# Performance work log

Hardware: AMD Instinct MI355X
Metric: run time of the kernel (lower is better)

The kernel has to match this reference:

```python
import jax, jax.numpy as jnp
import numpy as np

RADIUS = 5
KERNEL = 2 * RADIUS + 1  # 11
N_PATCHES = KERNEL * KERNEL  # 121
SIGMA_DIAG = np.array([10.0, 10.0, 0.02, 0.02, 0.02, 0.1, 0.1, 0.1], dtype=np.float32)


def _shift(x):
    # x: [B, C, H, W] -> [B, P, C, H, W] with P = KERNEL^2 reflect-padded window shifts
    b, c, h, w = x.shape
    xp = jnp.pad(x, ((0, 0), (0, 0), (RADIUS, RADIUS), (RADIUS, RADIUS)), mode='reflect')
    patches = [xp[:, :, dy:dy + h, dx:dx + w]
               for dy in range(KERNEL) for dx in range(KERNEL)]
    return jnp.stack(patches, axis=1)


def setup_inputs() -> dict:
    key = jax.random.key(0)
    k1, k2 = jax.random.split(key)
    image = jax.random.uniform(k1, (2, 3, 256, 256), dtype=jnp.float32)
    guidance = jax.random.uniform(k2, (2, 8, 256, 256), dtype=jnp.float32)
    return {"image": image, "guidance": guidance}


def reference(image, guidance):
    # sigma_inv = inverse of diag(SIGMA_DIAG): diagonal, so just reciprocal per channel
    sigma_inv = jnp.asarray(1.0 / SIGMA_DIAG, dtype=guidance.dtype)  # [8]

    sg = _shift(guidance)                       # [B, P, 8, H, W]
    center = sg[:, N_PATCHES // 2:N_PATCHES // 2 + 1]
    diff = sg - center                          # [B, P, 8, H, W]
    # Mahalanobis^2 with diagonal sigma_inv: sum_c diff^2 / sigma_c
    maha_sq = jnp.einsum('bpchw,c->bphw', diff * diff, sigma_inv)
    weights = jnp.exp(-0.5 * maha_sq)           # [B, P, H, W]

    si = _shift(image)                          # [B, P, 3, H, W]
    weighted_sum = jnp.einsum('bpchw,bphw->bchw', si, weights)
    sum_w = jnp.clip(jnp.sum(weights, axis=1, keepdims=False), 1e-10, None)  # [B, H, W]
    return weighted_sum / sum_w[:, None]        # [B, 3, H, W]
```

## Files before the change

### kernel.cpp

```cpp
#include <hip/hip_runtime.h>

#define RADIUS 5
#define KSIZE  11
#define TILEX  32
#define TILEY  16
#define HX     (TILEX + 2*RADIUS)
#define HY     (TILEY + 2*RADIUS)
#define HPITCH 21
#define H      256
#define W      256

#define COEF_A (-0.072134752f)
#define COEF_B (-36.06737602f)
#define COEF_C (-7.213475204f)

__device__ __forceinline__ float wcalc(const float4 a, const float4 g,
                                       const float4 cA, const float4 cB) {
    const float d0 = a.x - cA.x, d1 = a.y - cA.y;
    const float d2 = a.z - cA.z, d3 = a.w - cA.w;
    const float d4 = g.x - cB.x, d5 = g.y - cB.y;
    const float d6 = g.z - cB.z, d7 = g.w - cB.w;
    const float sA = d0 * d0 + d1 * d1;
    const float sB = d2 * d2 + d3 * d3 + d4 * d4;
    const float sC = d5 * d5 + d6 * d6 + d7 * d7;
    return __builtin_amdgcn_exp2f(COEF_A * sA + COEF_B * sB + COEF_C * sC);
}

__global__ __launch_bounds__(1024, 4) void jbf_kernel(
    const float* __restrict__ image,
    const float* __restrict__ guidance,
    float* __restrict__ out)
{
    __shared__ float4 g0e[HY * HPITCH], g0o[HY * HPITCH];
    __shared__ float4 g1e[HY * HPITCH], g1o[HY * HPITCH];
    __shared__ float4 ime[HY * HPITCH], imo[HY * HPITCH];

    const int b       = blockIdx.z;
    const int tile_x0 = blockIdx.x * TILEX;
    const int tile_y0 = blockIdx.y * TILEY;
    const int txp     = threadIdx.x;
    const int h       = threadIdx.y;
    const int typ     = threadIdx.z;
    const int tid     = (typ * 4 + h) * 16 + txp;

    const float* gbase = guidance + (size_t)b * 8 * H * W;
    const float* ibase = image    + (size_t)b * 3 * H * W;

    for (int idx = tid; idx < HX * HY; idx += 1024) {
        const int ly = idx / HX;
        const int lx = idx - ly * HX;
        int gy = tile_y0 - RADIUS + ly;
        int gx = tile_x0 - RADIUS + lx;
        gy = (gy < 0) ? -gy : ((gy >= H) ? 2 * (H - 1) - gy : gy);
        gx = (gx < 0) ? -gx : ((gx >= W) ? 2 * (W - 1) - gx : gx);
        const int off = gy * W + gx;
        const int l   = ly * HPITCH + (lx >> 1);
        const float4 v0 = make_float4(gbase[0*H*W+off], gbase[1*H*W+off],
                                      gbase[2*H*W+off], gbase[3*H*W+off]);
        const float4 v1 = make_float4(gbase[4*H*W+off], gbase[5*H*W+off],
                                      gbase[6*H*W+off], gbase[7*H*W+off]);
        const float4 vi = make_float4(ibase[0*H*W+off], ibase[1*H*W+off],
                                      ibase[2*H*W+off], 0.f);
        if (lx & 1) { g0o[l] = v0; g1o[l] = v1; imo[l] = vi; }
        else        { g0e[l] = v0; g1e[l] = v1; ime[l] = vi; }
    }
    __syncthreads();

    const int crow = (typ + RADIUS) * HPITCH;
    const float4 c0A = g0o[crow + txp + 2], c0B = g1o[crow + txp + 2];
    const float4 c1A = g0e[crow + txp + 3], c1B = g1e[crow + txp + 3];

    float a00 = 0.f, a01 = 0.f, a02 = 0.f, sw0 = 0.f;
    float a10 = 0.f, a11 = 0.f, a12 = 0.f, sw1 = 0.f;

    #pragma unroll
    for (int i = 0; i < 3; ++i) {
        const int dy = 4 * i + h;
        if (dy < KSIZE) {
            const int rb = (typ + dy) * HPITCH + txp;
            #pragma unroll
            for (int k = 0; k <= 5; ++k) {
                const float4 Eg0 = g0e[rb + k], Eg1 = g1e[rb + k], Eim = ime[rb + k];
                const float4 Og0 = g0o[rb + k], Og1 = g1o[rb + k], Oim = imo[rb + k];

                {
                    const float w = wcalc(Eg0, Eg1, c0A, c0B);
                    sw0 += w; a00 += w * Eim.x; a01 += w * Eim.y; a02 += w * Eim.z;
                }
                if (k <= 4) {
                    const float w = wcalc(Og0, Og1, c0A, c0B);
                    sw0 += w; a00 += w * Oim.x; a01 += w * Oim.y; a02 += w * Oim.z;
                }
                {
                    const float w = wcalc(Og0, Og1, c1A, c1B);
                    sw1 += w; a10 += w * Oim.x; a11 += w * Oim.y; a12 += w * Oim.z;
                }
                if (k >= 1) {
                    const float w = wcalc(Eg0, Eg1, c1A, c1B);
                    sw1 += w; a10 += w * Eim.x; a11 += w * Eim.y; a12 += w * Eim.z;
                }
            }
        }
    }

    sw0 += __shfl_xor(sw0, 16);  sw0 += __shfl_xor(sw0, 32);
    a00 += __shfl_xor(a00, 16);  a00 += __shfl_xor(a00, 32);
    a01 += __shfl_xor(a01, 16);  a01 += __shfl_xor(a01, 32);
    a02 += __shfl_xor(a02, 16);  a02 += __shfl_xor(a02, 32);
    sw1 += __shfl_xor(sw1, 16);  sw1 += __shfl_xor(sw1, 32);
    a10 += __shfl_xor(a10, 16);  a10 += __shfl_xor(a10, 32);
    a11 += __shfl_xor(a11, 16);  a11 += __shfl_xor(a11, 32);
    a12 += __shfl_xor(a12, 16);  a12 += __shfl_xor(a12, 32);

    if (h == 0) {
        const float inv0 = 1.0f / sw0;
        const float inv1 = 1.0f / sw1;
        const size_t o = (size_t)b * 3 * H * W + (size_t)(tile_y0 + typ) * W
                       + (size_t)(tile_x0 + 2 * txp);
        float2* __restrict__ o2 = (float2*)(out + o);
        o2[0]           = make_float2(a00 * inv0, a10 * inv1);
        o2[(H*W) / 2]   = make_float2(a01 * inv0, a11 * inv1);
        o2[(2*H*W) / 2] = make_float2(a02 * inv0, a12 * inv1);
    }
}

extern "C" void kernel_launch(void* const* d_in, const int* in_sizes, int n_in,
                              void* d_out, int out_size, void* d_ws, size_t ws_size,
                              hipStream_t stream) {
    const float* image    = (const float*)d_in[0];
    const float* guidance = (const float*)d_in[1];
    float* out            = (float*)d_out;

    const int B = in_sizes[0] / (3 * H * W);
    dim3 grid(W / TILEX, H / TILEY, B);
    dim3 block(16, 4, 16);
    hipLaunchKernelGGL(jbf_kernel, grid, block, 0, stream, image, guidance, out);
}
```

Baseline: 72.47 us.

## Expand squared distance algebraically and compute 2x2 output pixels per thread

Rewrites the Mahalanobis distance as phi(p) + phi(c) - 2 c·p, precomputing phi per halo pixel in the shared-memory image slot, so each weight becomes a dot product plus exp. Each thread now produces a 2x2 block of outputs (two rows), sharing shared-memory loads across vertical neighbours, with the block halved to 512 threads. Out-of-range rows are masked by multiplying with a 0/1 gate instead of branching, which adds some wasted exp work. The expansion can lose precision through cancellation when the large channel coefficients multiply values near each other.

```diff
diff --git a/kernel.cpp b/kernel.cpp
--- a/kernel.cpp
+++ b/kernel.cpp
@@ -1,7 +1,6 @@
 #include <hip/hip_runtime.h>
 
 #define RADIUS 5
-#define KSIZE  11
 #define TILEX  32
 #define TILEY  16
 #define HX     (TILEX + 2*RADIUS)
@@ -10,23 +9,23 @@
 #define H      256
 #define W      256
 
-#define COEF_A (-0.072134752f)
-#define COEF_B (-36.06737602f)
-#define COEF_C (-7.213475204f)
+#define KA (-0.072134752f)
+#define KB (-36.06737602f)
+#define KC (-7.213475204f)
 
-__device__ __forceinline__ float wcalc(const float4 a, const float4 g,
-                                       const float4 cA, const float4 cB) {
-    const float d0 = a.x - cA.x, d1 = a.y - cA.y;
-    const float d2 = a.z - cA.z, d3 = a.w - cA.w;
-    const float d4 = g.x - cB.x, d5 = g.y - cB.y;
-    const float d6 = g.z - cB.z, d7 = g.w - cB.w;
-    const float sA = d0 * d0 + d1 * d1;
-    const float sB = d2 * d2 + d3 * d3 + d4 * d4;
-    const float sC = d5 * d5 + d6 * d6 + d7 * d7;
-    return __builtin_amdgcn_exp2f(COEF_A * sA + COEF_B * sB + COEF_C * sC);
+struct Center { float4 hA, hB; float phic; };
+
+__device__ __forceinline__ void accum(const float4 A, const float4 G, const float4 P,
+                                      const Center& C, const float gate,
+                                      float& sw, float& ax, float& ay, float& az) {
+    const float t = P.w + C.phic
+                  + C.hA.x*A.x + C.hA.y*A.y + C.hA.z*A.z + C.hA.w*A.w
+                  + C.hB.x*G.x + C.hB.y*G.y + C.hB.z*G.z + C.hB.w*G.w;
+    const float w = gate * __builtin_amdgcn_exp2f(t);
+    sw += w; ax += w * P.x; ay += w * P.y; az += w * P.z;
 }
 
-__global__ __launch_bounds__(1024, 4) void jbf_kernel(
+__global__ __launch_bounds__(512, 2) void jbf_kernel(
     const float* __restrict__ image,
     const float* __restrict__ guidance,
     float* __restrict__ out)
@@ -46,7 +45,7 @@
     const float* gbase = guidance + (size_t)b * 8 * H * W;
     const float* ibase = image    + (size_t)b * 3 * H * W;
 
-    for (int idx = tid; idx < HX * HY; idx += 1024) {
+    for (int idx = tid; idx < HX * HY; idx += 512) {
         const int ly = idx / HX;
         const int lx = idx - ly * HX;
         int gy = tile_y0 - RADIUS + ly;
@@ -59,68 +58,90 @@
                                       gbase[2*H*W+off], gbase[3*H*W+off]);
         const float4 v1 = make_float4(gbase[4*H*W+off], gbase[5*H*W+off],
                                       gbase[6*H*W+off], gbase[7*H*W+off]);
+        const float phi = KA * (v0.x*v0.x + v0.y*v0.y)
+                        + KB * (v0.z*v0.z + v0.w*v0.w + v1.x*v1.x)
+                        + KC * (v1.y*v1.y + v1.z*v1.z + v1.w*v1.w);
         const float4 vi = make_float4(ibase[0*H*W+off], ibase[1*H*W+off],
-                                      ibase[2*H*W+off], 0.f);
+                                      ibase[2*H*W+off], phi);
         if (lx & 1) { g0o[l] = v0; g1o[l] = v1; imo[l] = vi; }
         else        { g0e[l] = v0; g1e[l] = v1; ime[l] = vi; }
     }
     __syncthreads();
 
-    const int crow = (typ + RADIUS) * HPITCH;
-    const float4 c0A = g0o[crow + txp + 2], c0B = g1o[crow + txp + 2];
-    const float4 c1A = g0e[crow + txp + 3], c1B = g1e[crow + txp + 3];
+    Center c[2][2];
+    #pragma unroll
+    for (int cy = 0; cy < 2; ++cy) {
+        const int row = (2 * typ + 5 + cy) * HPITCH;
+        #pragma unroll
+        for (int cx = 0; cx < 2; ++cx) {
+            const int ci = row + txp + 2 + cx;
+            const float4 gA = cx ? g0e[ci] : g0o[ci];
+            const float4 gB = cx ? g1e[ci] : g1o[ci];
+            const float4 pv = cx ? ime[ci] : imo[ci];
+            c[cx][cy].hA = make_float4(-2.f*KA*gA.x, -2.f*KA*gA.y,
+                                       -2.f*KB*gA.z, -2.f*KB*gA.w);
+            c[cx][cy].hB = make_float4(-2.f*KB*gB.x, -2.f*KC*gB.y,
+                                       -2.f*KC*gB.z, -2.f*KC*gB.w);
+            c[cx][cy].phic = pv.w;
+        }
+    }
 
-    float a00 = 0.f, a01 = 0.f, a02 = 0.f, sw0 = 0.f;
-    float a10 = 0.f, a11 = 0.f, a12 = 0.f, sw1 = 0.f;
+    float s[2][2]  = {{0.f,0.f},{0.f,0.f}};
+    float ax[2][2] = {{0.f,0.f},{0.f,0.f}};
+    float ay[2][2] = {{0.f,0.f},{0.f,0.f}};
+    float az[2][2] = {{0.f,0.f},{0.f,0.f}};
 
     #pragma unroll
     for (int i = 0; i < 3; ++i) {
-        const int dy = 4 * i + h;
-        if (dy < KSIZE) {
-            const int rb = (typ + dy) * HPITCH + txp;
-            #pragma unroll
-            for (int k = 0; k <= 5; ++k) {
-                const float4 Eg0 = g0e[rb + k], Eg1 = g1e[rb + k], Eim = ime[rb + k];
-                const float4 Og0 = g0o[rb + k], Og1 = g1o[rb + k], Oim = imo[rb + k];
-
-                {
-                    const float w = wcalc(Eg0, Eg1, c0A, c0B);
-                    sw0 += w; a00 += w * Eim.x; a01 += w * Eim.y; a02 += w * Eim.z;
+        const int r  = 4 * i + h;
+        const int rb = (2 * typ + r) * HPITCH + txp;
+        const float fy0 = (r <= 10) ? 1.0f : 0.0f;
+        const float fy1 = (r >= 1)  ? 1.0f : 0.0f;
+        #pragma unroll
+        for (int k = 0; k <= 5; ++k) {
+            {
+                const float4 A = g0e[rb + k], G = g1e[rb + k], P = ime[rb + k];
+                accum(A, G, P, c[0][0], fy0, s[0][0], ax[0][0], ay[0][0], az[0][0]);
+                accum(A, G, P, c[0][1], fy1, s[0][1], ax[0][1], ay[0][1], az[0][1]);
+                if (k >= 1) {
+                    accum(A, G, P, c[1][0], fy0, s[1][0], ax[1][0], ay[1][0], az[1][0]);
+                    accum(A, G, P, c[1][1], fy1, s[1][1], ax[1][1], ay[1][1], az[1][1]);
                 }
+            }
+            {
+                const float4 A = g0o[rb + k], G = g1o[rb + k], P = imo[rb + k];
                 if (k <= 4) {
-                    const float w = wcalc(Og0, Og1, c0A, c0B);
-                    sw0 += w; a00 += w * Oim.x; a01 += w * Oim.y; a02 += w * Oim.z;
+                    accum(A, G, P, c[0][0], fy0, s[0][0], ax[0][0], ay[0][0], az[0][0]);
+                    accum(A, G, P, c[0][1], fy1, s[0][1], ax[0][1], ay[0][1], az[0][1]);
                 }
-                {
-                    const float w = wcalc(Og0, Og1, c1A, c1B);
-                    sw1 += w; a10 += w * Oim.x; a11 += w * Oim.y; a12 += w * Oim.z;
-                }
-                if (k >= 1) {
-                    const float w = wcalc(Eg0, Eg1, c1A, c1B);
-                    sw1 += w; a10 += w * Eim.x; a11 += w * Eim.y; a12 += w * Eim.z;
-                }
+                accum(A, G, P, c[1][0], fy0, s[1][0], ax[1][0], ay[1][0], az[1][0]);
+                accum(A, G, P, c[1][1], fy1, s[1][1], ax[1][1], ay[1][1], az[1][1]);
             }
         }
     }
 
-    sw0 += __shfl_xor(sw0, 16);  sw0 += __shfl_xor(sw0, 32);
-    a00 += __shfl_xor(a00, 16);  a00 += __shfl_xor(a00, 32);
-    a01 += __shfl_xor(a01, 16);  a01 += __shfl_xor(a01, 32);
-    a02 += __shfl_xor(a02, 16);  a02 += __shfl_xor(a02, 32);
-    sw1 += __shfl_xor(sw1, 16);  sw1 += __shfl_xor(sw1, 32);
-    a10 += __shfl_xor(a10, 16);  a10 += __shfl_xor(a10, 32);
-    a11 += __shfl_xor(a11, 16);  a11 += __shfl_xor(a11, 32);
-    a12 += __shfl_xor(a12, 16);  a12 += __shfl_xor(a12, 32);
+    #pragma unroll
+    for (int cx = 0; cx < 2; ++cx)
+        #pragma unroll
+        for (int cy = 0; cy < 2; ++cy) {
+            s[cx][cy]  += __shfl_xor(s[cx][cy], 16);  s[cx][cy]  += __shfl_xor(s[cx][cy], 32);
+            ax[cx][cy] += __shfl_xor(ax[cx][cy], 16); ax[cx][cy] += __shfl_xor(ax[cx][cy], 32);
+            ay[cx][cy] += __shfl_xor(ay[cx][cy], 16); ay[cx][cy] += __shfl_xor(ay[cx][cy], 32);
+            az[cx][cy] += __shfl_xor(az[cx][cy], 16); az[cx][cy] += __shfl_xor(az[cx][cy], 32);
+        }
 
     if (h == 0) {
-        const float inv0 = 1.0f / sw0;
-        const float inv1 = 1.0f / sw1;
-        const size_t o = (size_t)b * 3 * H * W + (size_t)(tile_y0 + typ) * W
-                       + (size_t)(tile_x0 + 2 * txp);
-        float2* __restrict__ o2 = (float2*)(out + o);
-        o2[0]           = make_float2(a00 * inv0, a10 * inv1);
-        o2[(H*W) / 2]   = make_float2(a01 * inv0, a11 * inv1);
-        o2[(2*H*W) / 2] = make_float2(a02 * inv0, a12 * inv1);
+        const size_t base = (size_t)b * 3 * H * W
+                          + (size_t)(tile_y0 + 2 * typ) * W + (tile_x0 + 2 * txp);
+        #pragma unroll
+        for (int cy = 0; cy < 2; ++cy) {
+            const float i0 = 1.0f / s[0][cy];
+            const float i1 = 1.0f / s[1][cy];
+            float2* __restrict__ o2 = (float2*)(out + base + (size_t)cy * W);
+            o2[0]           = make_float2(ax[0][cy] * i0, ax[1][cy] * i1);
+            o2[(H*W) / 2]   = make_float2(ay[0][cy] * i0, ay[1][cy] * i1);
+            o2[(2*H*W) / 2] = make_float2(az[0][cy] * i0, az[1][cy] * i1);
+        }
     }
 }
 
@@ -133,6 +154,6 @@
 
     const int B = in_sizes[0] / (3 * H * W);
     dim3 grid(W / TILEX, H / TILEY, B);
-    dim3 block(16, 4, 16);
+    dim3 block(16, 4, 8);
     hipLaunchKernelGGL(jbf_kernel, grid, block, 0, stream, image, guidance, out);
 }
```

After: 71.62 us. About the same (-1.2%).
